# Performance work log

Measured on AMD Instinct MI355X. Metric: run time of the kernel, lower is better.

## Reference

```python
import jax, jax.numpy as jnp
import numpy as np

G, K, R = 33, 8, 8
B, HL, WL, HF, WF = 4, 256, 256, 1080, 1920


def setup_inputs() -> dict:
    key = jax.random.key(0)
    ks = jax.random.split(key, 14)

    def n(k, shape, std=0.05):
        return jax.random.normal(k, shape, jnp.float32) * std

    # identity LUT [G,G,G,3] + small noise per basis, clamped to [0,1]
    rg = jnp.linspace(0.0, 1.0, G)
    Rr, Gg, Bb = jnp.meshgrid(rg, rg, rg, indexing='ij')
    ident = jnp.stack([Rr, Gg, Bb], axis=-1)
    bases = jnp.clip(ident[None] + jax.random.normal(ks[0], (K, G, G, G, 3), jnp.float32) * 0.01, 0.0, 1.0)

    return {
        'img_lr': jax.random.uniform(ks[1], (B, 3, HL, WL), jnp.float32),
        'img_full': jax.random.uniform(ks[2], (B, 3, HF, WF), jnp.float32),
        'bases': bases,
        'wp_c1_w': n(ks[3], (16, 3, 3, 3)), 'wp_c1_b': jnp.zeros(16, jnp.float32),
        'wp_c2_w': n(ks[4], (32, 16, 3, 3)), 'wp_c2_b': jnp.zeros(32, jnp.float32),
        'wp_fc_w': n(ks[5], (K, 32)), 'wp_fc_b': jnp.ones(K, jnp.float32),  # bias init 1.0
        'rp_c1_w': n(ks[6], (16, 3, 3, 3)), 'rp_c1_b': jnp.zeros(16, jnp.float32),
        'rp_c2_w': n(ks[7], (32, 16, 3, 3)), 'rp_c2_b': jnp.zeros(32, jnp.float32),
        'rp_fcu_w': n(ks[8], (R * G, 32)), 'rp_fcu_b': jnp.zeros(R * G, jnp.float32),
        'rp_fcv_w': n(ks[9], (R * G, 32)), 'rp_fcv_b': jnp.zeros(R * G, jnp.float32),
        'rp_fcw_w': n(ks[10], (R * G, 32)), 'rp_fcw_b': jnp.zeros(R * G, jnp.float32),
        'rp_fcc_w': n(ks[11], (R * 3, 32), std=0.1), 'rp_fcc_b': jnp.zeros(R * 3, jnp.float32),  # std=0.1, zero bias
    }


def _conv(x, w, b):
    y = jax.lax.conv_general_dilated(x, w, (2, 2), ((1, 1), (1, 1)),
                                     dimension_numbers=('NCHW', 'OIHW', 'NCHW'))
    return y + b[None, :, None, None]


def _encode(x, c1w, c1b, c2w, c2b):
    h = jax.nn.relu(_conv(x, c1w, c1b))
    h = jax.nn.relu(_conv(h, c2w, c2b))
    return h.mean((2, 3))  # AdaptiveAvgPool2d(1) -> [B,32]


def _trilinear(img, lut):
    # img: [B,3,H,W] in [0,1]; lut: [B,G,G,G,3]
    b, _, h, w = img.shape
    g = lut.shape[1]
    xyz = jnp.clip(jnp.transpose(img, (0, 2, 3, 1)) * (g - 1), 0.0, g - 1 - 1e-6)  # [B,H,W,3]
    i0 = jnp.floor(xyz).astype(jnp.int32)
    x0, y0, z0 = i0[..., 0], i0[..., 1], i0[..., 2]
    x1 = jnp.minimum(x0 + 1, g - 1)
    y1 = jnp.minimum(y0 + 1, g - 1)
    z1 = jnp.minimum(z0 + 1, g - 1)
    d = xyz - i0.astype(xyz.dtype)
    xd, yd, zd = d[..., 0:1], d[..., 1:2], d[..., 2:3]  # [B,H,W,1]
    lut_flat = lut.reshape(b, g * g * g, 3)

    def gather(ix, iy, iz):
        idx = ((ix * g + iy) * g + iz).reshape(b, -1, 1)
        return jnp.take_along_axis(lut_flat, idx, axis=1).reshape(b, h, w, 3)

    c000 = gather(x0, y0, z0); c100 = gather(x1, y0, z0)
    c010 = gather(x0, y1, z0); c110 = gather(x1, y1, z0)
    c001 = gather(x0, y0, z1); c101 = gather(x1, y0, z1)
    c011 = gather(x0, y1, z1); c111 = gather(x1, y1, z1)
    c00 = c000 * (1 - xd) + c100 * xd
    c01 = c001 * (1 - xd) + c101 * xd
    c10 = c010 * (1 - xd) + c110 * xd
    c11 = c011 * (1 - xd) + c111 * xd
    c0 = c00 * (1 - yd) + c10 * yd
    c1 = c01 * (1 - yd) + c11 * yd
    out = c0 * (1 - zd) + c1 * zd
    return jnp.transpose(out, (0, 3, 1, 2))  # [B,3,H,W]


def reference(img_lr, img_full, bases,
              wp_c1_w, wp_c1_b, wp_c2_w, wp_c2_b, wp_fc_w, wp_fc_b,
              rp_c1_w, rp_c1_b, rp_c2_w, rp_c2_b,
              rp_fcu_w, rp_fcu_b, rp_fcv_w, rp_fcv_b,
              rp_fcw_w, rp_fcw_b, rp_fcc_w, rp_fcc_b):
    b = img_lr.shape[0]
    # WeightPredictor: raw unnormalized alpha [B,K]
    alpha = _encode(img_lr, wp_c1_w, wp_c1_b, wp_c2_w, wp_c2_b) @ wp_fc_w.T + wp_fc_b
    # ResidualPredictor (note: no softmax/tanh applied in the source forward)
    hr = _encode(img_lr, rp_c1_w, rp_c1_b, rp_c2_w, rp_c2_b)
    u = (hr @ rp_fcu_w.T + rp_fcu_b).reshape(b, R, G)
    v = (hr @ rp_fcv_w.T + rp_fcv_b).reshape(b, R, G)
    w_ = (hr @ rp_fcw_w.T + rp_fcw_b).reshape(b, R, G)
    c = (hr @ rp_fcc_w.T + rp_fcc_b).reshape(b, R, 3)
    # CP residual -> [B,G,G,G,3]
    delta = jnp.einsum('brx,bry,brz,brc->bxyzc', u, v, w_, c)
    # fuse bases with raw alpha and add residual
    L = jnp.einsum('bk,kxyzc->bxyzc', alpha, bases) + delta
    out = _trilinear(img_full, L)
    delta_norm = jnp.mean(jnp.abs(delta))
    return (out, alpha, delta, L, delta_norm)
```

## Files before the change

### kernel.cpp

```cpp
#include <hip/hip_runtime.h>
#include <stdint.h>

#define GN   33
#define GG   1089
#define GGG  35937
#define BATCH 4
#define HFULL 1080
#define WFULL 1920
#define NPIX (HFULL*WFULL)
#define NPIX4 (NPIX/4)

#define OUT_ALPHA 24883200
#define OUT_DELTA 24883232
#define OUT_L     25314476
#define OUT_DNORM 25745720

#define WS_LUT64B 0
#define WS_PART   2300000
#define WS_DN     2308192
#define NLUTBLK   132

typedef float  float4n __attribute__((ext_vector_type(4)));
typedef unsigned int uint4n __attribute__((ext_vector_type(4)));

__device__ __forceinline__ unsigned short f2bf(float f) {
    unsigned u = __float_as_uint(f);
    unsigned r = (u + 0x7fffu + ((u >> 16) & 1u)) >> 16;
    return (unsigned short)r;
}
__device__ __forceinline__ float bflo(unsigned u) { return __uint_as_float(u << 16); }
__device__ __forceinline__ float bfhi(unsigned u) { return __uint_as_float(u & 0xffff0000u); }

__global__ __launch_bounds__(256) void encoder_kernel(
    const float* __restrict__ img,
    const float* __restrict__ w1wp, const float* __restrict__ b1wp,
    const float* __restrict__ w2wp, const float* __restrict__ b2wp,
    const float* __restrict__ w1rp, const float* __restrict__ b1rp,
    const float* __restrict__ w2rp, const float* __restrict__ b2rp,
    float* __restrict__ ws)
{
    const int bi = blockIdx.x;
    const int enc = bi >> 7, b = (bi >> 5) & 3, rt = (bi >> 1) & 15, ct = bi & 1;
    const float* w1 = enc ? w1rp : w1wp;
    const float* b1 = enc ? b1rp : b1wp;
    const float* w2 = enc ? w2rp : w2wp;
    const float* b2 = enc ? b2rp : b2wp;
    __shared__ float simg[3][19][132];
    __shared__ float sh1[4][9][66];
    __shared__ float red[4][16];
    const float* imb = img + (size_t)b * 3 * 65536;
    const int tid = threadIdx.x;

    for (int l = tid; l < 3 * 19 * 131; l += 256) {
        const int c = l / (19 * 131);
        const int rem = l - c * (19 * 131);
        const int rw = rem / 131, cl = rem - rw * 131;
        const int gr = 16 * rt - 3 + rw, gc = 128 * ct - 3 + cl;
        float v = 0.f;
        if ((unsigned)gr < 256u && (unsigned)gc < 256u)
            v = imb[(c << 16) + (gr << 8) + gc];
        simg[c][rw][cl] = v;
    }
    __syncthreads();

    const int p = tid & 127, h = tid >> 7;
    const int prow = p >> 5, pcol = p & 31;
    float acc[16];
    #pragma unroll
    for (int o = 0; o < 16; ++o) acc[o] = b2[h * 16 + o];

    for (int cc0 = 0; cc0 < 16; cc0 += 4) {
        if (cc0) __syncthreads();
        for (int l = tid; l < 4 * 9 * 65; l += 256) {
            const int oc = l / (9 * 65);
            const int rem = l - oc * (9 * 65);
            const int r = rem / 65, cl = rem - r * 65;
            const int hrow = 8 * rt - 1 + r, hcol = 64 * ct - 1 + cl;
            float v = 0.f;
            if ((unsigned)hrow < 128u && (unsigned)hcol < 128u) {
                float a1 = b1[cc0 + oc];
                const float* wo = w1 + (cc0 + oc) * 27;
                #pragma unroll
                for (int c = 0; c < 3; ++c)
                    #pragma unroll
                    for (int ky = 0; ky < 3; ++ky)
                        #pragma unroll
                        for (int kx = 0; kx < 3; ++kx)
                            a1 += wo[c * 9 + ky * 3 + kx] * simg[c][2 * r + ky][2 * cl + kx];
                v = fmaxf(a1, 0.f);
            }
            sh1[oc][r][cl] = v;
        }
        __syncthreads();
        #pragma unroll
        for (int cc = 0; cc < 4; ++cc) {
            float vv[9];
            #pragma unroll
            for (int ky = 0; ky < 3; ++ky)
                #pragma unroll
                for (int kx = 0; kx < 3; ++kx)
                    vv[ky * 3 + kx] = sh1[cc][2 * prow + ky][2 * pcol + kx];
            #pragma unroll
            for (int o = 0; o < 16; ++o) {
                const float* wo = w2 + (h * 16 + o) * 144 + (cc0 + cc) * 9;
                #pragma unroll
                for (int k = 0; k < 9; ++k) acc[o] += wo[k] * vv[k];
            }
        }
    }
    const int lane = tid & 63, wv = tid >> 6;
    #pragma unroll
    for (int o = 0; o < 16; ++o) {
        float v = fmaxf(acc[o], 0.f);
        #pragma unroll
        for (int off = 32; off; off >>= 1) v += __shfl_down(v, off);
        if (lane == 0) red[wv][o] = v;
    }
    __syncthreads();
    if (tid < 32) {
        const int o = tid & 15, g = tid >> 4;
        const float s = red[g * 2][o] + red[g * 2 + 1][o];
        ws[WS_PART + ((enc * 4 + b) * 32 + (rt * 2 + ct)) * 32 + g * 16 + o] = s;
    }
}

__global__ __launch_bounds__(256) void lut_kernel(
    const float* __restrict__ bases,
    const float* __restrict__ wp_fc_w, const float* __restrict__ wp_fc_b,
    const float* __restrict__ fcu_w, const float* __restrict__ fcu_b,
    const float* __restrict__ fcv_w, const float* __restrict__ fcv_b,
    const float* __restrict__ fcw_w, const float* __restrict__ fcw_b,
    const float* __restrict__ fcc_w, const float* __restrict__ fcc_b,
    float* __restrict__ ws, float* __restrict__ dout)
{
    const int b = blockIdx.x & 3;
    const int x = blockIdx.x >> 2;
    const int x1 = min(x + 1, GN - 1);
    const int tid = threadIdx.x;
    __shared__ float mean[2][32];
    __shared__ float U[264], V[264], W[264], Cc[24], Al[8];
    __shared__ float Lp[2][GG * 3];

    if (tid < 64) {
        const int enc = tid >> 5, o = tid & 31;
        const float* pp = ws + WS_PART + (enc * 4 + b) * 1024 + o;
        float s = 0.f;
        #pragma unroll
        for (int i = 0; i < 32; ++i) s += pp[i * 32];
        mean[enc][o] = s * (1.f / 4096.f);
    }
    __syncthreads();
    for (int r = tid; r < 824; r += 256) {
        if (r < 8) {
            const float* row = wp_fc_w + r * 32;
            float a = wp_fc_b[r];
            #pragma unroll 8
            for (int q = 0; q < 32; ++q) a += row[q] * mean[0][q];
            Al[r] = a;
            dout[OUT_ALPHA + b * 8 + r] = a;
        } else if (r < 272) {
            const int jj = r - 8;
            const float* row = fcu_w + jj * 32;
            float a = fcu_b[jj];
            #pragma unroll 8
            for (int q = 0; q < 32; ++q) a += row[q] * mean[1][q];
            U[jj] = a;
        } else if (r < 536) {
            const int jj = r - 272;
            const float* row = fcv_w + jj * 32;
            float a = fcv_b[jj];
            #pragma unroll 8
            for (int q = 0; q < 32; ++q) a += row[q] * mean[1][q];
            V[jj] = a;
        } else if (r < 800) {
            const int jj = r - 536;
            const float* row = fcw_w + jj * 32;
            float a = fcw_b[jj];
            #pragma unroll 8
            for (int q = 0; q < 32; ++q) a += row[q] * mean[1][q];
            W[jj] = a;
        } else {
            const int jj = r - 800;
            const float* row = fcc_w + jj * 32;
            float a = fcc_b[jj];
            #pragma unroll 8
            for (int q = 0; q < 32; ++q) a += row[q] * mean[1][q];
            Cc[jj] = a;
        }
    }
    __syncthreads();

    float ux0[8], ux1[8], cr[8][3];
    #pragma unroll
    for (int r = 0; r < 8; ++r) {
        ux0[r] = U[r * GN + x];
        ux1[r] = U[r * GN + x1];
        cr[r][0] = Cc[r * 3 + 0];
        cr[r][1] = Cc[r * 3 + 1];
        cr[r][2] = Cc[r * 3 + 2];
    }

    float sum3 = 0.f;
    #pragma unroll
    for (int px = 0; px < 2; ++px) {
        const int xi = px ? x1 : x;
        for (int i = tid; i < GG; i += 256) {
            const int y = i / GN, z = i - y * GN;
            float d0 = 0.f, d1 = 0.f, d2 = 0.f;
            #pragma unroll
            for (int r = 0; r < 8; ++r) {
                const float t = (px ? ux1[r] : ux0[r]) * V[r * GN + y] * W[r * GN + z];
                d0 += t * cr[r][0];
                d1 += t * cr[r][1];
                d2 += t * cr[r][2];
            }
            float l0 = d0, l1 = d1, l2 = d2;
            const float* bp = bases + (size_t)(xi * GG + i) * 3;
            #pragma unroll
            for (int k = 0; k < 8; ++k) {
                const float a = Al[k];
                const float* bk = bp + (size_t)k * GGG * 3;
                l0 += a * bk[0];
                l1 += a * bk[1];
                l2 += a * bk[2];
            }
            Lp[px][i * 3 + 0] = l0;
            Lp[px][i * 3 + 1] = l1;
            Lp[px][i * 3 + 2] = l2;
            if (px == 0) {
                const size_t o3 = ((size_t)b * GGG + x * GG + i) * 3;
                dout[OUT_DELTA + o3 + 0] = d0;
                dout[OUT_DELTA + o3 + 1] = d1;
                dout[OUT_DELTA + o3 + 2] = d2;
                dout[OUT_L + o3 + 0] = l0;
                dout[OUT_L + o3 + 1] = l1;
                dout[OUT_L + o3 + 2] = l2;
                sum3 += fabsf(d0) + fabsf(d1) + fabsf(d2);
            }
        }
    }
    __syncthreads();

    for (int i = tid; i < GG; i += 256) {
        const int y = i / GN, z = i - y * GN;
        const int y1 = min(y + 1, GN - 1), z1 = min(z + 1, GN - 1);
        const int i00 = (y  * GN + z ) * 3, i01 = (y  * GN + z1) * 3;
        const int i10 = (y1 * GN + z ) * 3, i11 = (y1 * GN + z1) * 3;
        uint4 wr, wg, wb;
        #pragma unroll
        for (int c = 0; c < 3; ++c) {
            const unsigned w00 = (unsigned)f2bf(Lp[0][i00 + c]) | ((unsigned)f2bf(Lp[0][i01 + c]) << 16);
            const unsigned w01 = (unsigned)f2bf(Lp[0][i10 + c]) | ((unsigned)f2bf(Lp[0][i11 + c]) << 16);
            const unsigned w10 = (unsigned)f2bf(Lp[1][i00 + c]) | ((unsigned)f2bf(Lp[1][i01 + c]) << 16);
            const unsigned w11 = (unsigned)f2bf(Lp[1][i10 + c]) | ((unsigned)f2bf(Lp[1][i11 + c]) << 16);
            uint4& wv = c == 0 ? wr : (c == 1 ? wg : wb);
            wv.x = w00; wv.y = w01; wv.z = w10; wv.w = w11;
        }
        uint4* dst = (uint4*)((char*)ws + WS_LUT64B) + ((size_t)b * GGG + x * GG + i) * 4;
        dst[0] = wr; dst[1] = wg; dst[2] = wb;
    }

    #pragma unroll
    for (int off = 32; off; off >>= 1) sum3 += __shfl_down(sum3, off);
    __shared__ float s4[4];
    const int lane = tid & 63, wid = tid >> 6;
    if (!lane) s4[wid] = sum3;
    __syncthreads();
    if (!tid) ws[WS_DN + blockIdx.x] = s4[0] + s4[1] + s4[2] + s4[3];
}

__global__ __launch_bounds__(256, 4) void apply_kernel(
    const float* __restrict__ img,
    const float* __restrict__ ws, float* __restrict__ dout)
{
    __shared__ float so[3 * 1093];

    if (blockIdx.x == 0 && threadIdx.x < 64) {
        float s = 0.f;
        for (int i = threadIdx.x; i < NLUTBLK; i += 64) s += ws[WS_DN + i];
        #pragma unroll
        for (int off = 32; off; off >>= 1) s += __shfl_down(s, off);
        if (threadIdx.x == 0)
            dout[OUT_DNORM] = s * (1.0f / (float)(BATCH * GGG * 3));
    }
    const int b = blockIdx.x & 3;
    const int tid = threadIdx.x;
    const int q = (blockIdx.x >> 2) * 256 + tid;
    const float4n* base = (const float4n*)(img + (size_t)b * 3 * NPIX);
    const float4n rv = __builtin_nontemporal_load(&base[q]);
    const float4n gv = __builtin_nontemporal_load(&base[NPIX4 + q]);
    const float4n bv = __builtin_nontemporal_load(&base[2 * NPIX4 + q]);
    const uint4* lut = (const uint4*)((const char*)ws + WS_LUT64B) + (size_t)b * GGG * 4;

    float rrr[4] = {rv.x, rv.y, rv.z, rv.w};
    float ggg[4] = {gv.x, gv.y, gv.z, gv.w};
    float bbb[4] = {bv.x, bv.y, bv.z, bv.w};
    int idx[4]; float xd[4], yd[4], zd[4];
    #pragma unroll
    for (int t = 0; t < 4; ++t) {
        const float xf = fminf(fmaxf(rrr[t] * 32.f, 0.f), 31.999998f);
        const float yf = fminf(fmaxf(ggg[t] * 32.f, 0.f), 31.999998f);
        const float zf = fminf(fmaxf(bbb[t] * 32.f, 0.f), 31.999998f);
        const int x0 = (int)xf, y0 = (int)yf, z0 = (int)zf;
        xd[t] = xf - (float)x0; yd[t] = yf - (float)y0; zd[t] = zf - (float)z0;
        idx[t] = (x0 * GN + y0) * GN + z0;
    }

    const int sub = tid & 3;
    const int qd  = tid >> 2;
    #pragma unroll
    for (int r = 0; r < 16; ++r) {
        const int src = r >> 2, sl = r & 3;
        const int   pidx = __shfl(idx[sl], src, 4);
        const float pxd  = __shfl(xd[sl],  src, 4);
        const float pyd  = __shfl(yd[sl],  src, 4);
        const float pzd  = __shfl(zd[sl],  src, 4);
        const uint4 e = lut[(size_t)(unsigned)pidx * 4 + sub];
        const float e0l = bflo(e.x), e1l = bflo(e.y), e2l = bflo(e.z), e3l = bflo(e.w);
        const float z00 = e0l + pzd * (bfhi(e.x) - e0l);
        const float z01 = e1l + pzd * (bfhi(e.y) - e1l);
        const float z10 = e2l + pzd * (bfhi(e.z) - e2l);
        const float z11 = e3l + pzd * (bfhi(e.w) - e3l);
        const float y0v = z00 + pyd * (z01 - z00);
        const float y1v = z10 + pyd * (z11 - z10);
        const float ov  = y0v + pxd * (y1v - y0v);
        if (sub < 3) so[sub * 1093 + qd * 17 + r] = ov;
    }
    __syncthreads();

    const int pb = 4 * tid + qd;
    float4n s0, s1, s2;
    s0.x = so[pb + 0];        s0.y = so[pb + 1];        s0.z = so[pb + 2];        s0.w = so[pb + 3];
    s1.x = so[1093 + pb + 0]; s1.y = so[1093 + pb + 1]; s1.z = so[1093 + pb + 2]; s1.w = so[1093 + pb + 3];
    s2.x = so[2186 + pb + 0]; s2.y = so[2186 + pb + 1]; s2.z = so[2186 + pb + 2]; s2.w = so[2186 + pb + 3];

    float4n* ob = (float4n*)(dout + (size_t)b * 3 * NPIX);
    __builtin_nontemporal_store(s0, &ob[q]);
    __builtin_nontemporal_store(s1, &ob[NPIX4 + q]);
    __builtin_nontemporal_store(s2, &ob[2 * NPIX4 + q]);
}

extern "C" void kernel_launch(void* const* d_in, const int* in_sizes, int n_in,
                              void* d_out, int out_size, void* d_ws, size_t ws_size,
                              hipStream_t stream)
{
    const float* img_lr   = (const float*)d_in[0];
    const float* img_full = (const float*)d_in[1];
    const float* bases    = (const float*)d_in[2];
    const float* wp_c1_w  = (const float*)d_in[3];
    const float* wp_c1_b  = (const float*)d_in[4];
    const float* wp_c2_w  = (const float*)d_in[5];
    const float* wp_c2_b  = (const float*)d_in[6];
    const float* wp_fc_w  = (const float*)d_in[7];
    const float* wp_fc_b  = (const float*)d_in[8];
    const float* rp_c1_w  = (const float*)d_in[9];
    const float* rp_c1_b  = (const float*)d_in[10];
    const float* rp_c2_w  = (const float*)d_in[11];
    const float* rp_c2_b  = (const float*)d_in[12];
    const float* fcu_w    = (const float*)d_in[13];
    const float* fcu_b    = (const float*)d_in[14];
    const float* fcv_w    = (const float*)d_in[15];
    const float* fcv_b    = (const float*)d_in[16];
    const float* fcw_w    = (const float*)d_in[17];
    const float* fcw_b    = (const float*)d_in[18];
    const float* fcc_w    = (const float*)d_in[19];
    const float* fcc_b    = (const float*)d_in[20];
    float* ws  = (float*)d_ws;
    float* out = (float*)d_out;

    encoder_kernel<<<dim3(256), 256, 0, stream>>>(
        img_lr, wp_c1_w, wp_c1_b, wp_c2_w, wp_c2_b,
        rp_c1_w, rp_c1_b, rp_c2_w, rp_c2_b, ws);
    lut_kernel<<<dim3(NLUTBLK), 256, 0, stream>>>(
        bases, wp_fc_w, wp_fc_b, fcu_w, fcu_b, fcv_w, fcv_b,
        fcw_w, fcw_b, fcc_w, fcc_b, ws, out);
    apply_kernel<<<dim3(BATCH * NPIX4 / 256), 256, 0, stream>>>(img_full, ws, out);
}
```

Measured before the change: 309.7 us.

## Stage pixel params in LDS and batch LUT gathers in two groups

In the apply kernel, the per-pixel LUT index and fractional weights are now written to shared memory and read back in bulk, instead of being broadcast with four cross-lane shuffles per pixel. The 16 LUT gathers per thread are issued as two batches of eight independent loads before the interpolation math, so more memory requests are in flight at once. The output staging buffer is re-padded to a 20-float stride so the final reads become aligned float4 loads. This costs about 16 KB of extra LDS, an extra barrier and more live registers, which may lower occupancy.

Result: no change. 309.9 us (+0.1%).

```diff
diff --git a/kernel.cpp b/kernel.cpp
--- a/kernel.cpp
+++ b/kernel.cpp
@@ -273,7 +273,8 @@
     const float* __restrict__ img,
     const float* __restrict__ ws, float* __restrict__ dout)
 {
-    __shared__ float so[3 * 1093];
+    __shared__ __align__(16) unsigned spbuf[16 * 64 * 4];
+    __shared__ __align__(16) float so[3 * 1304 + 8];
 
     if (blockIdx.x == 0 && threadIdx.x < 64) {
         float s = 0.f;
@@ -285,6 +286,8 @@
     }
     const int b = blockIdx.x & 3;
     const int tid = threadIdx.x;
+    const int sub = tid & 3;
+    const int qd  = tid >> 2;
     const int q = (blockIdx.x >> 2) * 256 + tid;
     const float4n* base = (const float4n*)(img + (size_t)b * 3 * NPIX);
     const float4n rv = __builtin_nontemporal_load(&base[q]);
@@ -295,44 +298,75 @@
     float rrr[4] = {rv.x, rv.y, rv.z, rv.w};
     float ggg[4] = {gv.x, gv.y, gv.z, gv.w};
     float bbb[4] = {bv.x, bv.y, bv.z, bv.w};
-    int idx[4]; float xd[4], yd[4], zd[4];
+    uint4n* spv = (uint4n*)spbuf;
     #pragma unroll
     for (int t = 0; t < 4; ++t) {
         const float xf = fminf(fmaxf(rrr[t] * 32.f, 0.f), 31.999998f);
         const float yf = fminf(fmaxf(ggg[t] * 32.f, 0.f), 31.999998f);
         const float zf = fminf(fmaxf(bbb[t] * 32.f, 0.f), 31.999998f);
         const int x0 = (int)xf, y0 = (int)yf, z0 = (int)zf;
-        xd[t] = xf - (float)x0; yd[t] = yf - (float)y0; zd[t] = zf - (float)z0;
-        idx[t] = (x0 * GN + y0) * GN + z0;
-    }
-
-    const int sub = tid & 3;
-    const int qd  = tid >> 2;
-    #pragma unroll
-    for (int r = 0; r < 16; ++r) {
-        const int src = r >> 2, sl = r & 3;
-        const int   pidx = __shfl(idx[sl], src, 4);
-        const float pxd  = __shfl(xd[sl],  src, 4);
-        const float pyd  = __shfl(yd[sl],  src, 4);
-        const float pzd  = __shfl(zd[sl],  src, 4);
-        const uint4 e = lut[(size_t)(unsigned)pidx * 4 + sub];
-        const float e0l = bflo(e.x), e1l = bflo(e.y), e2l = bflo(e.z), e3l = bflo(e.w);
-        const float z00 = e0l + pzd * (bfhi(e.x) - e0l);
-        const float z01 = e1l + pzd * (bfhi(e.y) - e1l);
-        const float z10 = e2l + pzd * (bfhi(e.z) - e2l);
-        const float z11 = e3l + pzd * (bfhi(e.w) - e3l);
+        uint4n pk;
+        pk.x = (unsigned)((x0 * GN + y0) * GN + z0);
+        pk.y = __float_as_uint(xf - (float)x0);
+        pk.z = __float_as_uint(yf - (float)y0);
+        pk.w = __float_as_uint(zf - (float)z0);
+        spv[(sub * 4 + t) * 64 + qd] = pk;
+    }
+    __syncthreads();
+
+    uint4n pr[8];
+    #pragma unroll
+    for (int j = 0; j < 8; ++j) pr[j] = spv[j * 64 + qd];
+    uint4 e[8];
+    #pragma unroll
+    for (int j = 0; j < 8; ++j)
+        e[j] = lut[(size_t)(pr[j].x * 4u + (unsigned)sub)];
+    uint4n pr2[8];
+    #pragma unroll
+    for (int j = 0; j < 8; ++j) pr2[j] = spv[(8 + j) * 64 + qd];
+
+    #pragma unroll
+    for (int j = 0; j < 8; ++j) {
+        const float pxd = __uint_as_float(pr[j].y);
+        const float pyd = __uint_as_float(pr[j].z);
+        const float pzd = __uint_as_float(pr[j].w);
+        const uint4 ee = e[j];
+        const float e0l = bflo(ee.x), e1l = bflo(ee.y), e2l = bflo(ee.z), e3l = bflo(ee.w);
+        const float z00 = e0l + pzd * (bfhi(ee.x) - e0l);
+        const float z01 = e1l + pzd * (bfhi(ee.y) - e1l);
+        const float z10 = e2l + pzd * (bfhi(ee.z) - e2l);
+        const float z11 = e3l + pzd * (bfhi(ee.w) - e3l);
         const float y0v = z00 + pyd * (z01 - z00);
         const float y1v = z10 + pyd * (z11 - z10);
         const float ov  = y0v + pxd * (y1v - y0v);
-        if (sub < 3) so[sub * 1093 + qd * 17 + r] = ov;
-    }
-    __syncthreads();
-
-    const int pb = 4 * tid + qd;
-    float4n s0, s1, s2;
-    s0.x = so[pb + 0];        s0.y = so[pb + 1];        s0.z = so[pb + 2];        s0.w = so[pb + 3];
-    s1.x = so[1093 + pb + 0]; s1.y = so[1093 + pb + 1]; s1.z = so[1093 + pb + 2]; s1.w = so[1093 + pb + 3];
-    s2.x = so[2186 + pb + 0]; s2.y = so[2186 + pb + 1]; s2.z = so[2186 + pb + 2]; s2.w = so[2186 + pb + 3];
+        if (sub < 3) so[sub * 1304 + qd * 20 + j] = ov;
+    }
+    uint4 e2[8];
+    #pragma unroll
+    for (int j = 0; j < 8; ++j)
+        e2[j] = lut[(size_t)(pr2[j].x * 4u + (unsigned)sub)];
+    #pragma unroll
+    for (int j = 0; j < 8; ++j) {
+        const float pxd = __uint_as_float(pr2[j].y);
+        const float pyd = __uint_as_float(pr2[j].z);
+        const float pzd = __uint_as_float(pr2[j].w);
+        const uint4 ee = e2[j];
+        const float e0l = bflo(ee.x), e1l = bflo(ee.y), e2l2 = bflo(ee.z), e3l = bflo(ee.w);
+        const float z00 = e0l + pzd * (bfhi(ee.x) - e0l);
+        const float z01 = e1l + pzd * (bfhi(ee.y) - e1l);
+        const float z10 = e2l2 + pzd * (bfhi(ee.z) - e2l2);
+        const float z11 = e3l + pzd * (bfhi(ee.w) - e3l);
+        const float y0v = z00 + pyd * (z01 - z00);
+        const float y1v = z10 + pyd * (z11 - z10);
+        const float ov  = y0v + pxd * (y1v - y0v);
+        if (sub < 3) so[sub * 1304 + qd * 20 + 8 + j] = ov;
+    }
+    __syncthreads();
+
+    const int pbase = 4 * tid + qd * 4;
+    const float4n s0 = *(const float4n*)&so[pbase];
+    const float4n s1 = *(const float4n*)&so[1304 + pbase];
+    const float4n s2 = *(const float4n*)&so[2608 + pbase];
 
     float4n* ob = (float4n*)(dout + (size_t)b * 3 * NPIX);
     __builtin_nontemporal_store(s0, &ob[q]);
```

## Switch LUT and interpolation to packed fp16 math with LDS-staged pixel params

Applied to the files above, without the earlier changes.

Stores the precomputed LUT corner pairs as packed fp16 instead of bf16 and performs the z and y interpolation steps with packed half2 FMA. Per-pixel index and fractional weights are packed into LDS instead of being passed through lane shuffles, and the gathers are batched eight at a time to increase memory-level parallelism. Outputs are staged through LDS as packed halves, which reduces LDS footprint, and the occupancy hint is raised to 5 blocks. The fp16 arithmetic and fp16 staging of outputs add rounding error, and LUT values outside the fp16 range or precision could exceed tolerance.

Result: slower. 316.7 us (+2.3%).

```diff
diff --git a/kernel.cpp b/kernel.cpp
--- a/kernel.cpp
+++ b/kernel.cpp
@@ -1,4 +1,5 @@
 #include <hip/hip_runtime.h>
+#include <hip/hip_fp16.h>
 #include <stdint.h>
 
 #define GN   33
@@ -23,13 +24,11 @@
 typedef float  float4n __attribute__((ext_vector_type(4)));
 typedef unsigned int uint4n __attribute__((ext_vector_type(4)));
 
-__device__ __forceinline__ unsigned short f2bf(float f) {
-    unsigned u = __float_as_uint(f);
-    unsigned r = (u + 0x7fffu + ((u >> 16) & 1u)) >> 16;
-    return (unsigned short)r;
-}
-__device__ __forceinline__ float bflo(unsigned u) { return __uint_as_float(u << 16); }
-__device__ __forceinline__ float bfhi(unsigned u) { return __uint_as_float(u & 0xffff0000u); }
+__device__ __forceinline__ __half2 u2h2(unsigned u) { union { unsigned u; __half2 h; } v; v.u = u; return v.h; }
+__device__ __forceinline__ unsigned h22u(__half2 h) { union { unsigned u; __half2 h; } v; v.h = h; return v.u; }
+__device__ __forceinline__ unsigned short h2u16(__half h) { union { __half h; unsigned short s; } v; v.h = h; return v.s; }
+__device__ __forceinline__ __half u162h(unsigned short s) { union { __half h; unsigned short s; } v; v.s = s; return v.h; }
+__device__ __forceinline__ unsigned packh2(float a, float b) { return h22u(__floats2half2_rn(a, b)); }
 
 __global__ __launch_bounds__(256) void encoder_kernel(
     const float* __restrict__ img,
@@ -246,18 +245,16 @@
         const int y1 = min(y + 1, GN - 1), z1 = min(z + 1, GN - 1);
         const int i00 = (y  * GN + z ) * 3, i01 = (y  * GN + z1) * 3;
         const int i10 = (y1 * GN + z ) * 3, i11 = (y1 * GN + z1) * 3;
-        uint4 wr, wg, wb;
+        uint4* dst = (uint4*)((char*)ws + WS_LUT64B) + ((size_t)b * GGG + x * GG + i) * 4;
         #pragma unroll
         for (int c = 0; c < 3; ++c) {
-            const unsigned w00 = (unsigned)f2bf(Lp[0][i00 + c]) | ((unsigned)f2bf(Lp[0][i01 + c]) << 16);
-            const unsigned w01 = (unsigned)f2bf(Lp[0][i10 + c]) | ((unsigned)f2bf(Lp[0][i11 + c]) << 16);
-            const unsigned w10 = (unsigned)f2bf(Lp[1][i00 + c]) | ((unsigned)f2bf(Lp[1][i01 + c]) << 16);
-            const unsigned w11 = (unsigned)f2bf(Lp[1][i10 + c]) | ((unsigned)f2bf(Lp[1][i11 + c]) << 16);
-            uint4& wv = c == 0 ? wr : (c == 1 ? wg : wb);
-            wv.x = w00; wv.y = w01; wv.z = w10; wv.w = w11;
-        }
-        uint4* dst = (uint4*)((char*)ws + WS_LUT64B) + ((size_t)b * GGG + x * GG + i) * 4;
-        dst[0] = wr; dst[1] = wg; dst[2] = wb;
+            uint4 wv;
+            wv.x = packh2(Lp[0][i00 + c], Lp[0][i10 + c]);
+            wv.y = packh2(Lp[0][i01 + c], Lp[0][i11 + c]);
+            wv.z = packh2(Lp[1][i00 + c], Lp[1][i10 + c]);
+            wv.w = packh2(Lp[1][i01 + c], Lp[1][i11 + c]);
+            dst[c] = wv;
+        }
     }
 
     #pragma unroll
@@ -269,11 +266,12 @@
     if (!tid) ws[WS_DN + blockIdx.x] = s4[0] + s4[1] + s4[2] + s4[3];
 }
 
-__global__ __launch_bounds__(256, 4) void apply_kernel(
+__global__ __launch_bounds__(256, 5) void apply_kernel(
     const float* __restrict__ img,
     const float* __restrict__ ws, float* __restrict__ dout)
 {
-    __shared__ float so[3 * 1093];
+    __shared__ __align__(16) uint2 sp[16 * 64];
+    __shared__ __align__(16) unsigned so[64 * 26];
 
     if (blockIdx.x == 0 && threadIdx.x < 64) {
         float s = 0.f;
@@ -285,6 +283,8 @@
     }
     const int b = blockIdx.x & 3;
     const int tid = threadIdx.x;
+    const int sub = tid & 3;
+    const int qd  = tid >> 2;
     const int q = (blockIdx.x >> 2) * 256 + tid;
     const float4n* base = (const float4n*)(img + (size_t)b * 3 * NPIX);
     const float4n rv = __builtin_nontemporal_load(&base[q]);
@@ -295,44 +295,66 @@
     float rrr[4] = {rv.x, rv.y, rv.z, rv.w};
     float ggg[4] = {gv.x, gv.y, gv.z, gv.w};
     float bbb[4] = {bv.x, bv.y, bv.z, bv.w};
-    int idx[4]; float xd[4], yd[4], zd[4];
     #pragma unroll
     for (int t = 0; t < 4; ++t) {
         const float xf = fminf(fmaxf(rrr[t] * 32.f, 0.f), 31.999998f);
         const float yf = fminf(fmaxf(ggg[t] * 32.f, 0.f), 31.999998f);
         const float zf = fminf(fmaxf(bbb[t] * 32.f, 0.f), 31.999998f);
         const int x0 = (int)xf, y0 = (int)yf, z0 = (int)zf;
-        xd[t] = xf - (float)x0; yd[t] = yf - (float)y0; zd[t] = zf - (float)z0;
-        idx[t] = (x0 * GN + y0) * GN + z0;
-    }
-
-    const int sub = tid & 3;
-    const int qd  = tid >> 2;
-    #pragma unroll
-    for (int r = 0; r < 16; ++r) {
-        const int src = r >> 2, sl = r & 3;
-        const int   pidx = __shfl(idx[sl], src, 4);
-        const float pxd  = __shfl(xd[sl],  src, 4);
-        const float pyd  = __shfl(yd[sl],  src, 4);
-        const float pzd  = __shfl(zd[sl],  src, 4);
-        const uint4 e = lut[(size_t)(unsigned)pidx * 4 + sub];
-        const float e0l = bflo(e.x), e1l = bflo(e.y), e2l = bflo(e.z), e3l = bflo(e.w);
-        const float z00 = e0l + pzd * (bfhi(e.x) - e0l);
-        const float z01 = e1l + pzd * (bfhi(e.y) - e1l);
-        const float z10 = e2l + pzd * (bfhi(e.z) - e2l);
-        const float z11 = e3l + pzd * (bfhi(e.w) - e3l);
-        const float y0v = z00 + pyd * (z01 - z00);
-        const float y1v = z10 + pyd * (z11 - z10);
-        const float ov  = y0v + pxd * (y1v - y0v);
-        if (sub < 3) so[sub * 1093 + qd * 17 + r] = ov;
-    }
-    __syncthreads();
-
-    const int pb = 4 * tid + qd;
+        const float xd = xf - (float)x0, yd = yf - (float)y0, zd = zf - (float)z0;
+        uint2 pk;
+        pk.x = (unsigned)((x0 * GN + y0) * GN + z0) |
+               ((unsigned)h2u16(__float2half_rn(xd)) << 16);
+        pk.y = packh2(yd, zd);
+        sp[(sub * 4 + t) * 64 + qd] = pk;
+    }
+    __syncthreads();
+
+    #pragma unroll
+    for (int h = 0; h < 2; ++h) {
+        uint2 pr[8];
+        #pragma unroll
+        for (int j = 0; j < 8; ++j) pr[j] = sp[(h * 8 + j) * 64 + qd];
+        uint4 e[8];
+        #pragma unroll
+        for (int j = 0; j < 8; ++j)
+            e[j] = lut[(size_t)(pr[j].x & 0xffffu) * 4u + (unsigned)sub];
+        float ov[8];
+        #pragma unroll
+        for (int j = 0; j < 8; ++j) {
+            const float pxd = __half2float(u162h((unsigned short)(pr[j].x >> 16)));
+            const __half2 yz = u2h2(pr[j].y);
+            const __half2 yd2 = __low2half2(yz), zd2 = __high2half2(yz);
+            const uint4 ee = e[j];
+            const __half2 w0 = u2h2(ee.x), w1 = u2h2(ee.y);
+            const __half2 w2 = u2h2(ee.z), w3 = u2h2(ee.w);
+            const __half2 z01 = __hfma2(zd2, __hsub2(w1, w0), w0);
+            const __half2 z23 = __hfma2(zd2, __hsub2(w3, w2), w2);
+            const unsigned A = __byte_perm(h22u(z01), h22u(z23), 0x5410);
+            const unsigned B = __byte_perm(h22u(z01), h22u(z23), 0x7632);
+            const __half2 hA = u2h2(A);
+            const __half2 Y = __hfma2(yd2, __hsub2(u2h2(B), hA), hA);
+            const float y0v = __low2float(Y), y1v = __high2float(Y);
+            ov[j] = fmaf(pxd, y1v - y0v, y0v);
+            if ((j & 1) && sub < 3) {
+                const int jp = h * 4 + (j >> 1);
+                so[qd * 26 + jp * 3 + sub] = packh2(ov[j - 1], ov[j]);
+            }
+        }
+    }
+    __syncthreads();
+
+    const int st = qd * 26 + 6 * sub;
+    const uint2 u0 = *(const uint2*)&so[st];
+    const uint2 u1 = *(const uint2*)&so[st + 2];
+    const uint2 u2 = *(const uint2*)&so[st + 4];
     float4n s0, s1, s2;
-    s0.x = so[pb + 0];        s0.y = so[pb + 1];        s0.z = so[pb + 2];        s0.w = so[pb + 3];
-    s1.x = so[1093 + pb + 0]; s1.y = so[1093 + pb + 1]; s1.z = so[1093 + pb + 2]; s1.w = so[1093 + pb + 3];
-    s2.x = so[2186 + pb + 0]; s2.y = so[2186 + pb + 1]; s2.z = so[2186 + pb + 2]; s2.w = so[2186 + pb + 3];
+    s0.x = __low2float(u2h2(u0.x)); s0.y = __high2float(u2h2(u0.x));
+    s0.z = __low2float(u2h2(u1.y)); s0.w = __high2float(u2h2(u1.y));
+    s1.x = __low2float(u2h2(u0.y)); s1.y = __high2float(u2h2(u0.y));
+    s1.z = __low2float(u2h2(u2.x)); s1.w = __high2float(u2h2(u2.x));
+    s2.x = __low2float(u2h2(u1.x)); s2.y = __high2float(u2h2(u1.x));
+    s2.z = __low2float(u2h2(u2.y)); s2.w = __high2float(u2h2(u2.y));
 
     float4n* ob = (float4n*)(dout + (size_t)b * 3 * NPIX);
     __builtin_nontemporal_store(s0, &ob[q]);
```
